# Kernel optimization log

Hardware: AMD Instinct MI355X
Metric: run time of the kernel (lower is better)

## Reference

```python
import jax, jax.numpy as jnp
import numpy as np

# Module config (matches init_kwargs)
P_THRESH = 0.9
IOU_THRESH = 0.5
WIDTH, HEIGHT = 3072, 2304
NUM_PATCHES = 96
XPS = WIDTH // NUM_PATCHES   # 32, math.floor(width / num_of_patches)
YPS = HEIGHT // NUM_PATCHES  # 24


def setup_inputs() -> dict:
    key = jax.random.key(0)
    x = jax.random.uniform(key, (5, NUM_PATCHES, NUM_PATCHES), dtype=jnp.float32)
    return {"x": x}


def reference(x):
    """Fixed-shape JAX version of ReduceBoundingBoxes.forward.

    Returns out: [N, 5] rows (score, x, y, w, h) sorted by descending score;
    rows not surviving (prob threshold + greedy NMS) are zeroed.
    (Torch returns only the kept rows; here kept rows appear first, in the
    same order, with identical values, followed by zero rows.)
    """
    P, Q = x.shape[1], x.shape[2]
    N = P * Q
    dt = x.dtype
    ii = (jnp.arange(P, dtype=dt) * XPS)[:, None]  # i * x_patch_size
    jj = (jnp.arange(Q, dtype=dt) * YPS)[None, :]  # j * y_patch_size

    prob = x[0]
    # convert_batch_bbx_to_xyxy_scaled (applied everywhere; only rows passing
    # the prob threshold survive, identical to torch's masked in-place update)
    bx1 = x[1] * WIDTH + ii
    by1 = x[2] * HEIGHT + jj
    bx2 = (x[3] - x[1]) * WIDTH + ii
    by2 = (x[4] - x[2]) * HEIGHT + jj

    boxes = jnp.stack([bx1, by1, bx2, by2], axis=-1).reshape(N, 4)
    scores = prob.reshape(N)
    valid = scores > P_THRESH

    # Sort by descending score; invalid boxes sink to the end.
    order = jnp.argsort(-jnp.where(valid, scores, -jnp.inf))
    boxes_s = boxes[order]
    scores_s = scores[order]
    valid_s = valid[order]

    x1, y1, x2, y2 = boxes_s[:, 0], boxes_s[:, 1], boxes_s[:, 2], boxes_s[:, 3]
    area = (x2 - x1) * (y2 - y1)
    # Pairwise IoU (torchvision convention, no +1). [N, N] -- dominant buffer.
    iw = jnp.clip(jnp.minimum(x2[:, None], x2[None, :]) - jnp.maximum(x1[:, None], x1[None, :]), 0.0)
    ih = jnp.clip(jnp.minimum(y2[:, None], y2[None, :]) - jnp.maximum(y1[:, None], y1[None, :]), 0.0)
    inter = iw * ih
    iou = inter / (area[:, None] + area[None, :] - inter + 1e-9)

    # Greedy NMS: sequential suppression in score order.
    idx = jnp.arange(N)

    def body(i, keep):
        sup = keep[i] & (iou[i] > IOU_THRESH) & (idx > i)
        return keep & ~sup

    keep = jax.lax.fori_loop(0, N, body, valid_s)

    # convert_batch_to_xywh on (score, x1, y1, x2, y2)
    out = jnp.stack([scores_s, x1, y1, x2 - x1, y2 - y1], axis=-1)
    out = jnp.where(keep[:, None], out, jnp.zeros((), dtype=dt))
    return out
```

## Files before the change

### kernel.cpp

```cpp
#pragma clang fp contract(off)
#include <hip/hip_runtime.h>

#define NP 96
#define N_TOT (NP * NP)
#define FWIDTH 3072.0f
#define FHEIGHT 2304.0f
#define XPS 32
#define YPS 24
#define VMAX 1024
typedef unsigned long long u64;

#define WS_MSK   0
#define WS_RANK  131072
#define WS_FLAGS 135168
#define MAGIC(b) (0x5AD0F00Du ^ (unsigned)(b))

__global__ __launch_bounds__(1024)
void k_one(const float* __restrict__ x, float* __restrict__ out,
           u64* __restrict__ msk, unsigned int* __restrict__ grank,
           unsigned int* __restrict__ flags) {
    __shared__ u64 lk[VMAX];
    __shared__ float qx1[VMAX], qy1[VMAX], qx2[VMAX], qy2[VMAX], qa[VMAX];
    __shared__ int part[1024];
    __shared__ unsigned int wcnt[16];
    __shared__ u64 savail[16], sD[16];

    const int t = threadIdx.x;
    const int lane = t & 63;
    const int wid = t >> 6;
    const int bid = blockIdx.x;

    const int rbase = wid * 576;
    unsigned int cw = 0;
    for (int i = 0; i < 9; ++i) {
        float s = x[rbase + (i << 6) + lane];
        cw += (unsigned int)__popcll(__ballot(s > 0.9f));
    }
    if (lane == 0) wcnt[wid] = cw;
    __syncthreads();
    unsigned int off = 0, tot = 0;
    #pragma unroll
    for (int w = 0; w < 16; ++w) { if (w < wid) off += wcnt[w]; tot += wcnt[w]; }
    const int V = (tot > VMAX) ? VMAX : (int)tot;

    const u64 below = (lane == 0) ? 0ull : (~0ull >> (64 - lane));
    unsigned int base = off;
    for (int i = 0; i < 9; ++i) {
        const int n = rbase + (i << 6) + lane;
        const float s = x[n];
        const bool v = s > 0.9f;
        const u64 m = __ballot(v ? 1 : 0);
        if (v) {
            unsigned int pos = base + (unsigned int)__popcll(m & below);
            if (pos < VMAX) {
                unsigned int bits = __float_as_uint(s);
                lk[pos] = ((u64)(~bits) << 32) | (unsigned int)n;
            }
        }
        base += (unsigned int)__popcll(m);
    }
    for (int i = V + t; i < VMAX; i += 1024) lk[i] = ~0ULL;
    __syncthreads();

    {
        float bx1 = 0.f, by1 = 0.f, bx2 = 0.f, by2 = 0.f, ar = 0.f;
        if (t < V) {
            u64 key = lk[t];
            unsigned int n = (unsigned int)(key & 0xffffffffu);
            int pi = (int)n / NP, pj = (int)n % NP;
            float fi = (float)(pi * XPS);
            float fj = (float)(pj * YPS);
            float v1 = x[1 * N_TOT + n];
            float v2 = x[2 * N_TOT + n];
            float v3 = x[3 * N_TOT + n];
            float v4 = x[4 * N_TOT + n];
            bx1 = __fadd_rn(__fmul_rn(v1, FWIDTH), fi);
            by1 = __fadd_rn(__fmul_rn(v2, FHEIGHT), fj);
            bx2 = __fadd_rn(__fmul_rn(__fsub_rn(v3, v1), FWIDTH), fi);
            by2 = __fadd_rn(__fmul_rn(__fsub_rn(v4, v2), FHEIGHT), fj);
            ar  = __fmul_rn(__fsub_rn(bx2, bx1), __fsub_rn(by2, by1));
        }
        qx1[t] = bx1; qy1[t] = by1; qx2[t] = bx2; qy2[t] = by2; qa[t] = ar;
    }
    const int p = (bid << 6) + lane;
    const u64 colkey = lk[p];
    {
        int c = 0;
        const int sb = wid << 6;
        #pragma unroll 8
        for (int k = 0; k < 64; ++k)
            c += (lk[sb + k] < colkey) ? 1 : 0;
        part[t] = c;
    }
    __syncthreads();

    {
        const float bx1 = qx1[p], by1 = qy1[p], bx2 = qx2[p], by2 = qy2[p], ba = qa[p];
        const int ib = wid << 6;
        u64 bits = 0ull;
        #pragma unroll 4
        for (int m = 0; m < 64; ++m) {
            const int im = ib + m;
            float iw = fmaxf(__fsub_rn(fminf(qx2[im], bx2), fmaxf(qx1[im], bx1)), 0.0f);
            float ih = fmaxf(__fsub_rn(fminf(qy2[im], by2), fmaxf(qy1[im], by1)), 0.0f);
            float inter = __fmul_rn(iw, ih);
            float denom = __fadd_rn(__fsub_rn(__fadd_rn(qa[im], ba), inter), 1e-9f);
            bool pred = (lk[im] < colkey) && ((inter / denom) > 0.5f);
            bits |= ((u64)(pred ? 1u : 0u)) << m;
        }
        msk[(wid << 10) + p] = bits;
    }
    if (t < 64 && p < V) {
        int rank = 0;
        #pragma unroll
        for (int sg = 0; sg < 16; ++sg) rank += part[lane + (sg << 6)];
        grank[p] = (unsigned int)rank;
    }
    if (bid > 0) {
        const int gt = ((bid - 1) << 10) + t;
        for (int i = VMAX * 5 + gt; i < N_TOT * 5; i += 15360) out[i] = 0.0f;
    }
    __syncthreads();
    __threadfence();
    if (t == 0) atomicExch(&flags[bid], MAGIC(bid));
    if (bid != 0) return;

    if (t == 0) {
        for (int b = 0; b < 16; ++b)
            while (atomicAdd(&flags[b], 0u) != MAGIC(b)) { __builtin_amdgcn_s_sleep(1); }
    }
    __syncthreads();
    __threadfence();

    const bool valid = (t < V);
    u64 colw[16];
    #pragma unroll
    for (int c = 0; c < 16; ++c)
        colw[c] = msk[(c << 10) + t];

    u64 w0 = __ballot(valid ? 1 : 0);
    if (lane == 0) savail[wid] = w0;
    __syncthreads();

    bool kept = false;
    for (;;) {
        u64 av[16]; u64 any = 0ull;
        #pragma unroll
        for (int c = 0; c < 16; ++c) { av[c] = savail[c]; any |= av[c]; }
        if (any == 0ull) break;
        const bool in_avail = valid && ((av[wid] >> lane) & 1ull);
        u64 conf = 0ull;
        #pragma unroll
        for (int c = 0; c < 16; ++c) conf |= (colw[c] & av[c]);
        const bool isD = in_avail && (conf == 0ull);
        u64 Dw = __ballot(isD ? 1 : 0);
        if (lane == 0) sD[wid] = Dw;
        __syncthreads();
        u64 confD = 0ull;
        #pragma unroll
        for (int c = 0; c < 16; ++c) confD |= (colw[c] & sD[c]);
        if (isD) kept = true;
        const bool drop = in_avail && (isD || confD != 0ull);
        u64 dropw = __ballot(drop ? 1 : 0);
        if (lane == 0) savail[wid] = av[wid] & ~dropw;
        __syncthreads();
    }

    if (valid) {
        unsigned int r = grank[t];
        float o0 = 0.f, o1 = 0.f, o2 = 0.f, o3 = 0.f, o4 = 0.f;
        if (kept) {
            u64 key = lk[t];
            o0 = __uint_as_float(~(unsigned int)(key >> 32));
            o1 = qx1[t];
            o2 = qy1[t];
            o3 = __fsub_rn(qx2[t], qx1[t]);
            o4 = __fsub_rn(qy2[t], qy1[t]);
        }
        out[r * 5 + 0] = o0;
        out[r * 5 + 1] = o1;
        out[r * 5 + 2] = o2;
        out[r * 5 + 3] = o3;
        out[r * 5 + 4] = o4;
    } else {
        out[t * 5 + 0] = 0.f;
        out[t * 5 + 1] = 0.f;
        out[t * 5 + 2] = 0.f;
        out[t * 5 + 3] = 0.f;
        out[t * 5 + 4] = 0.f;
    }
}

extern "C" void kernel_launch(void* const* d_in, const int* in_sizes, int n_in,
                              void* d_out, int out_size, void* d_ws, size_t ws_size,
                              hipStream_t stream) {
    const float* x = (const float*)d_in[0];
    float* out = (float*)d_out;
    char* ws = (char*)d_ws;
    u64*          msk   = (u64*)(ws + WS_MSK);
    unsigned int* grank = (unsigned int*)(ws + WS_RANK);
    unsigned int* flags = (unsigned int*)(ws + WS_FLAGS);

    hipLaunchKernelGGL(k_one, dim3(16), dim3(1024), 0, stream,
                       x, out, msk, grank, flags);
}
```

Before: 87.03 us.

## Split fused kernel into build and resolve launches instead of spin-wait grid sync

```diff
diff --git a/kernel.cpp b/kernel.cpp
--- a/kernel.cpp
+++ b/kernel.cpp
@@ -12,18 +12,24 @@
 
 #define WS_MSK   0
 #define WS_RANK  131072
-#define WS_FLAGS 135168
-#define MAGIC(b) (0x5AD0F00Du ^ (unsigned)(b))
+#define WS_CNT   135168
+#define WS_BX1   135232
+#define WS_BY1   139328
+#define WS_BX2   143424
+#define WS_BY2   147520
+#define WS_SSC   151616
 
 __global__ __launch_bounds__(1024)
-void k_one(const float* __restrict__ x, float* __restrict__ out,
-           u64* __restrict__ msk, unsigned int* __restrict__ grank,
-           unsigned int* __restrict__ flags) {
+void k_build(const float* __restrict__ x, float* __restrict__ out,
+             u64* __restrict__ msk, unsigned int* __restrict__ grank,
+             unsigned int* __restrict__ cntp,
+             float* __restrict__ gbx1, float* __restrict__ gby1,
+             float* __restrict__ gbx2, float* __restrict__ gby2,
+             float* __restrict__ gssc) {
     __shared__ u64 lk[VMAX];
     __shared__ float qx1[VMAX], qy1[VMAX], qx2[VMAX], qy2[VMAX], qa[VMAX];
     __shared__ int part[1024];
     __shared__ unsigned int wcnt[16];
-    __shared__ u64 savail[16], sD[16];
 
     const int t = threadIdx.x;
     const int lane = t & 63;
@@ -116,23 +122,34 @@
         for (int sg = 0; sg < 16; ++sg) rank += part[lane + (sg << 6)];
         grank[p] = (unsigned int)rank;
     }
-    if (bid > 0) {
-        const int gt = ((bid - 1) << 10) + t;
-        for (int i = VMAX * 5 + gt; i < N_TOT * 5; i += 15360) out[i] = 0.0f;
-    }
-    __syncthreads();
-    __threadfence();
-    if (t == 0) atomicExch(&flags[bid], MAGIC(bid));
-    if (bid != 0) return;
-
-    if (t == 0) {
-        for (int b = 0; b < 16; ++b)
-            while (atomicAdd(&flags[b], 0u) != MAGIC(b)) { __builtin_amdgcn_s_sleep(1); }
-    }
-    __syncthreads();
-    __threadfence();
-
+    {
+        const int gt = (bid << 10) + t;
+        for (int i = VMAX * 5 + gt; i < N_TOT * 5; i += 16384) out[i] = 0.0f;
+    }
+    if (bid == 0) {
+        if (t == 0) *cntp = (unsigned int)V;
+        gbx1[t] = qx1[t];
+        gby1[t] = qy1[t];
+        gbx2[t] = qx2[t];
+        gby2[t] = qy2[t];
+        gssc[t] = __uint_as_float(~(unsigned int)(lk[t] >> 32));
+    }
+}
+
+__global__ __launch_bounds__(1024)
+void k_resolve(const unsigned int* __restrict__ cntp,
+               const u64* __restrict__ msk, const unsigned int* __restrict__ grank,
+               const float* __restrict__ gbx1, const float* __restrict__ gby1,
+               const float* __restrict__ gbx2, const float* __restrict__ gby2,
+               const float* __restrict__ gssc, float* __restrict__ out) {
+    __shared__ u64 savail[16], sD[16];
+    const int t = threadIdx.x;
+    const int lane = t & 63;
+    const int wid = t >> 6;
+    const int V = (int)*cntp;
     const bool valid = (t < V);
+
+    const float x1 = gbx1[t], y1 = gby1[t], x2 = gbx2[t], y2 = gby2[t], sc = gssc[t];
     u64 colw[16];
     #pragma unroll
     for (int c = 0; c < 16; ++c)
@@ -170,12 +187,11 @@
         unsigned int r = grank[t];
         float o0 = 0.f, o1 = 0.f, o2 = 0.f, o3 = 0.f, o4 = 0.f;
         if (kept) {
-            u64 key = lk[t];
-            o0 = __uint_as_float(~(unsigned int)(key >> 32));
-            o1 = qx1[t];
-            o2 = qy1[t];
-            o3 = __fsub_rn(qx2[t], qx1[t]);
-            o4 = __fsub_rn(qy2[t], qy1[t]);
+            o0 = sc;
+            o1 = x1;
+            o2 = y1;
+            o3 = __fsub_rn(x2, x1);
+            o4 = __fsub_rn(y2, y1);
         }
         out[r * 5 + 0] = o0;
         out[r * 5 + 1] = o1;
@@ -199,8 +215,15 @@
     char* ws = (char*)d_ws;
     u64*          msk   = (u64*)(ws + WS_MSK);
     unsigned int* grank = (unsigned int*)(ws + WS_RANK);
-    unsigned int* flags = (unsigned int*)(ws + WS_FLAGS);
-
-    hipLaunchKernelGGL(k_one, dim3(16), dim3(1024), 0, stream,
-                       x, out, msk, grank, flags);
+    unsigned int* cnt   = (unsigned int*)(ws + WS_CNT);
+    float* gbx1 = (float*)(ws + WS_BX1);
+    float* gby1 = (float*)(ws + WS_BY1);
+    float* gbx2 = (float*)(ws + WS_BX2);
+    float* gby2 = (float*)(ws + WS_BY2);
+    float* gssc = (float*)(ws + WS_SSC);
+
+    hipLaunchKernelGGL(k_build,   dim3(16), dim3(1024), 0, stream,
+                       x, out, msk, grank, cnt, gbx1, gby1, gbx2, gby2, gssc);
+    hipLaunchKernelGGL(k_resolve, dim3(1),  dim3(1024), 0, stream,
+                       cnt, msk, grank, gbx1, gby1, gbx2, gby2, gssc, out);
 }
```

New measurement: 79.70 us. 8.4% less time.
